# Performance work log

Hardware: AMD Instinct MI355X
Metric: run time of the kernel (lower is better)

Reference implementation:

```python
import jax, jax.numpy as jnp
import numpy as np

N, E, D, H = 20000, 320000, 128, 256
N_ITER = 3

def _w(k, fi, fo):
    return jax.random.normal(k, (fi, fo), jnp.float32) / np.sqrt(fi)

def setup_inputs() -> dict:
    key = jax.random.key(0)
    ks = jax.random.split(key, 16)
    inp = {
        "x": jax.random.normal(ks[0], (N, D), jnp.float32),
        "edge_attr": jax.random.normal(ks[1], (E, D), jnp.float32),
        "edge_index": jax.random.randint(ks[2], (2, E), 0, N, jnp.int32),
        # EASP edge encoder: cat[src,tgt,edge] (3D) -> H -> D
        "enc_w1": _w(ks[3], 3 * D, H), "enc_b1": jnp.zeros((H,), jnp.float32),
        "enc_w2": _w(ks[4], H, D), "enc_b2": jnp.zeros((D,), jnp.float32),
        # EdgeCNN: cat[src(2D), tgt(2D), edge(2D)] = 6D -> H -> D (reattach doubles dims)
        "em_w1": _w(ks[5], 6 * D, H), "em_b1": jnp.zeros((H,), jnp.float32),
        "em_w2": _w(ks[6], H, D), "em_b2": jnp.zeros((D,), jnp.float32),
        # node message MLP: cat[x_src(2D), edge(D)] = 3D -> H -> D
        "nm_w1": _w(ks[7], 3 * D, H), "nm_b1": jnp.zeros((H,), jnp.float32),
        "nm_w2": _w(ks[8], H, D), "nm_b2": jnp.zeros((D,), jnp.float32),
        # node output linear after aggregation
        "no_w": _w(ks[9], D, D), "no_b": jnp.zeros((D,), jnp.float32),
        # shared LayerNorms (ModuleList([layer]*n_iter) shares params)
        "node_ln_g": jnp.ones((D,), jnp.float32), "node_ln_b": jnp.zeros((D,), jnp.float32),
        "edge_ln_g": jnp.ones((D,), jnp.float32), "edge_ln_b": jnp.zeros((D,), jnp.float32),
    }
    return inp

def _ln(v, g, b):
    mu = jnp.mean(v, axis=-1, keepdims=True)
    var = jnp.mean(jnp.square(v - mu), axis=-1, keepdims=True)
    return (v - mu) * jax.lax.rsqrt(var + 1e-5) * g + b

def _mlp2(v, w1, b1, w2, b2):
    return jnp.maximum(v @ w1 + b1, 0.0) @ w2 + b2

def reference(x, edge_attr, edge_index,
              enc_w1, enc_b1, enc_w2, enc_b2,
              em_w1, em_b1, em_w2, em_b2,
              nm_w1, nm_b1, nm_w2, nm_b2,
              no_w, no_b, node_ln_g, node_ln_b, edge_ln_g, edge_ln_b):
    src, tgt = edge_index[0], edge_index[1]
    # edge encoder (EASP)
    init_edge = _mlp2(jnp.concatenate([x[src], x[tgt], edge_attr], axis=1),
                      enc_w1, enc_b1, enc_w2, enc_b2)  # [E, D]
    node_f, edge_f = x, init_edge
    deg = jax.ops.segment_sum(jnp.ones((E,), jnp.float32), tgt, num_segments=N)
    inv_deg = 1.0 / jnp.maximum(deg, 1.0)  # [N]
    for _ in range(N_ITER):
        node_c = jnp.concatenate([x, node_f], axis=1)          # [N, 2D] reattach
        edge_c = jnp.concatenate([init_edge, edge_f], axis=1)  # [E, 2D] reattach
        # edge update
        edge_f = _mlp2(jnp.concatenate([node_c[src], node_c[tgt], edge_c], axis=1),
                       em_w1, em_b1, em_w2, em_b2)             # [E, D]
        # node update: message -> scatter-mean -> linear
        msg = _mlp2(jnp.concatenate([node_c[src], edge_f], axis=1),
                    nm_w1, nm_b1, nm_w2, nm_b2)                # [E, D]
        agg = jax.ops.segment_sum(msg, tgt, num_segments=N) * inv_deg[:, None]
        node_f = agg @ no_w + no_b                             # [N, D]
        # residual + shared LayerNorm
        node_f = _ln(x + node_f, node_ln_g, node_ln_b)
        edge_f = _ln(init_edge + edge_f, edge_ln_g, edge_ln_b)
    return node_f, edge_f
```

## Files before the change

kernel.cpp:

```cpp
#include <hip/hip_runtime.h>
#include <stdint.h>

#define NN 20000
#define NE 320000
#define DD 128
#define HH 256
#define EB 48
#define EBE 64

using ushort8 = __attribute__((ext_vector_type(8))) unsigned short;
using bf16x8  = __attribute__((ext_vector_type(8))) __bf16;
using floatx4 = __attribute__((ext_vector_type(4))) float;

__device__ __forceinline__ unsigned short f2bf(float f) {
  union { float f; uint32_t u; } c; c.f = f;
  uint32_t u = c.u;
  return (unsigned short)((u + 0x7FFFu + ((u >> 16) & 1u)) >> 16);
}
__device__ __forceinline__ float bf2f(unsigned short h) {
  union { uint32_t u; float f; } c; c.u = ((uint32_t)h) << 16;
  return c.f;
}
__device__ __forceinline__ bf16x8 ld_bf8(const unsigned short* p) {
  ushort8 t = *(const ushort8*)p;
  return __builtin_bit_cast(bf16x8, t);
}
__device__ __forceinline__ void split8(const float* p, bf16x8& hi, bf16x8& lo) {
  floatx4 f0 = *(const floatx4*)p;
  floatx4 f1 = *(const floatx4*)(p + 4);
  ushort8 h, l;
#pragma unroll
  for (int k = 0; k < 4; ++k) {
    unsigned short a = f2bf(f0[k]);
    h[k] = a; l[k] = f2bf(f0[k] - bf2f(a));
    unsigned short b = f2bf(f1[k]);
    h[k+4] = b; l[k+4] = f2bf(f1[k] - bf2f(b));
  }
  hi = __builtin_bit_cast(bf16x8, h);
  lo = __builtin_bit_cast(bf16x8, l);
}
__device__ __forceinline__ floatx4 MFMA3(bf16x8 ah, bf16x8 al, bf16x8 bh, bf16x8 bl, floatx4 c) {
  c = __builtin_amdgcn_mfma_f32_16x16x32_bf16(ah, bh, c, 0, 0, 0);
  c = __builtin_amdgcn_mfma_f32_16x16x32_bf16(al, bh, c, 0, 0, 0);
  c = __builtin_amdgcn_mfma_f32_16x16x32_bf16(ah, bl, c, 0, 0, 0);
  return c;
}


__global__ void wconv_kernel(const float* __restrict__ in,
                             unsigned short* __restrict__ out_hi,
                             unsigned short* __restrict__ out_lo,
                             int K, int Nc) {
  int i = blockIdx.x * 256 + threadIdx.x;
  if (i >= K * Nc) return;
  int k = i / Nc, n = i - k * Nc;
  float v = in[i];
  unsigned short h = f2bf(v);
  out_hi[(size_t)n * K + k] = h;
  out_lo[(size_t)n * K + k] = f2bf(v - bf2f(h));
}

__global__ void xconv_kernel(const float* __restrict__ x,
                             unsigned short* __restrict__ xh, unsigned short* __restrict__ xl,
                             unsigned short* __restrict__ nh, unsigned short* __restrict__ nl) {
  int i = blockIdx.x * 256 + threadIdx.x;
  if (i < NN * DD) {
    float v = x[i];
    unsigned short h = f2bf(v), l = f2bf(v - bf2f(h));
    xh[i] = h; xl[i] = l; nh[i] = h; nl[i] = l;
  }
}

__global__ void deg_kernel(const int* __restrict__ ei, float* __restrict__ deg) {
  int e = blockIdx.x * 256 + threadIdx.x;
  if (e < NE) atomicAdd(&deg[ei[NE + e]], 1.0f);
}

__global__ void inv_kernel(const float* __restrict__ deg, float* __restrict__ idg) {
  int n = blockIdx.x * 256 + threadIdx.x;
  if (n < NN) idg[n] = 1.0f / fmaxf(deg[n], 1.0f);
}


template<int NCH, bool USE_NF>
__launch_bounds__(256, 2)
__global__ void nodepre_kernel(
    const unsigned short* __restrict__ xh, const unsigned short* __restrict__ xl,
    const unsigned short* __restrict__ nh, const unsigned short* __restrict__ nl,
    const unsigned short* __restrict__ w0h, const unsigned short* __restrict__ w0l,
    int ko0, int st0, float* __restrict__ out0,
    const unsigned short* __restrict__ w1h, const unsigned short* __restrict__ w1l,
    int ko1, int st1, float* __restrict__ out1,
    const unsigned short* __restrict__ w2h, const unsigned short* __restrict__ w2l,
    int ko2, int st2, float* __restrict__ out2)
{
  const int y = blockIdx.y;
  const unsigned short* Wh = (y == 0) ? w0h : (y == 1) ? w1h : w2h;
  const unsigned short* Wl = (y == 0) ? w0l : (y == 1) ? w1l : w2l;
  const int ko = (y == 0) ? ko0 : (y == 1) ? ko1 : ko2;
  const int st = (y == 0) ? st0 : (y == 1) ? st1 : st2;
  float* out = (y == 0) ? out0 : (y == 1) ? out1 : out2;

  const int tid = threadIdx.x;
  const int n0 = blockIdx.x * 64;
  const int lane = tid & 63, wv = tid >> 6;
  const int lr = lane & 15, kg = lane >> 4;
  int nr[4];
#pragma unroll
  for (int rt = 0; rt < 4; ++rt) {
    const int n = n0 + rt*16 + lr;
    nr[rt] = (n < NN) ? n : (NN - 1);
  }
  const floatx4 Z4 = {0.f, 0.f, 0.f, 0.f};
  floatx4 acc[4][4];
#pragma unroll
  for (int i = 0; i < 4; ++i)
#pragma unroll
    for (int j = 0; j < 4; ++j) acc[i][j] = Z4;

#pragma unroll
  for (int ch = 0; ch < NCH; ++ch) {
    bf16x8 ah[4], al[4], bh[4], bl[4];
#pragma unroll
    for (int rt = 0; rt < 4; ++rt) {
      if (USE_NF && ch >= 4) {
        const size_t off = (size_t)nr[rt] * DD + (ch - 4)*32 + kg*8;
        ah[rt] = ld_bf8(nh + off); al[rt] = ld_bf8(nl + off);
      } else {
        const size_t off = (size_t)nr[rt] * DD + ch*32 + kg*8;
        ah[rt] = ld_bf8(xh + off); al[rt] = ld_bf8(xl + off);
      }
    }
#pragma unroll
    for (int ct = 0; ct < 4; ++ct) {
      const size_t wo = (size_t)(wv*64 + ct*16 + lr) * st + ko + ch*32 + kg*8;
      bh[ct] = ld_bf8(Wh + wo); bl[ct] = ld_bf8(Wl + wo);
    }
#pragma unroll
    for (int rt = 0; rt < 4; ++rt)
#pragma unroll
      for (int ct = 0; ct < 4; ++ct) acc[rt][ct] = MFMA3(ah[rt], al[rt], bh[ct], bl[ct], acc[rt][ct]);
  }
#pragma unroll
  for (int ct = 0; ct < 4; ++ct) {
    const int col = wv*64 + ct*16 + lr;
#pragma unroll
    for (int rt = 0; rt < 4; ++rt)
#pragma unroll
      for (int j = 0; j < 4; ++j) {
        const int n = n0 + rt*16 + kg*4 + j;
        if (n < NN) out[(size_t)n * HH + col] = acc[rt][ct][j];
      }
  }
}


__launch_bounds__(256, 2)
__global__ void encoder_kernel(
    const float* __restrict__ ea,
    const int* __restrict__ ei,
    const float* __restrict__ pes,
    const float* __restrict__ pet,
    const unsigned short* __restrict__ w1h, const unsigned short* __restrict__ w1l,
    const float* __restrict__ b1,
    const unsigned short* __restrict__ w2h, const unsigned short* __restrict__ w2l,
    const float* __restrict__ b2,
    float* __restrict__ ief32, float* __restrict__ eff32)
{
  __shared__ unsigned short h_hi[EBE * 264];
  __shared__ unsigned short h_lo[EBE * 264];
  __shared__ int sidx[EBE];
  __shared__ int tidx[EBE];
  const int tid = threadIdx.x;
  const int e0 = blockIdx.x * EBE;
  if (tid < EBE) { sidx[tid] = ei[e0 + tid]; tidx[tid] = ei[NE + e0 + tid]; }
  __syncthreads();

  const int lane = tid & 63, wv = tid >> 6;
  const int lr = lane & 15, kg = lane >> 4;
  const floatx4 Z4 = {0.f, 0.f, 0.f, 0.f};

  float pse[4][4][4];
#pragma unroll
  for (int rt = 0; rt < 4; ++rt)
#pragma unroll
    for (int j = 0; j < 4; ++j) {
      const int row = rt*16 + kg*4 + j;
      const float* ps = pes + (size_t)sidx[row] * HH;
      const float* pt = pet + (size_t)tidx[row] * HH;
#pragma unroll
      for (int ct = 0; ct < 4; ++ct) {
        const int col = wv*64 + ct*16 + lr;
        pse[rt][j][ct] = ps[col] + pt[col];
      }
    }

  floatx4 acc[4][4];
#pragma unroll
  for (int i = 0; i < 4; ++i)
#pragma unroll
    for (int j = 0; j < 4; ++j) acc[i][j] = Z4;
#pragma unroll
  for (int sub = 0; sub < 4; ++sub) {
    const int off = sub*32 + kg*8;
    bf16x8 ah[4], al[4], bh[4], bl[4];
#pragma unroll
    for (int rt = 0; rt < 4; ++rt)
      split8(ea + (size_t)(e0 + rt*16 + lr) * DD + off, ah[rt], al[rt]);
#pragma unroll
    for (int ct = 0; ct < 4; ++ct) {
      const size_t wo = (size_t)(wv*64 + ct*16 + lr) * 384 + 256 + off;
      bh[ct] = ld_bf8(w1h + wo); bl[ct] = ld_bf8(w1l + wo);
    }
#pragma unroll
    for (int rt = 0; rt < 4; ++rt)
#pragma unroll
      for (int ct = 0; ct < 4; ++ct) acc[rt][ct] = MFMA3(ah[rt], al[rt], bh[ct], bl[ct], acc[rt][ct]);
  }
#pragma unroll
  for (int ct = 0; ct < 4; ++ct) {
    const int col = wv*64 + ct*16 + lr;
    const float bias = b1[col];
#pragma unroll
    for (int rt = 0; rt < 4; ++rt)
#pragma unroll
      for (int j = 0; j < 4; ++j) {
        const float v = fmaxf(acc[rt][ct][j] + bias + pse[rt][j][ct], 0.f);
        const unsigned short hh = f2bf(v);
        const int idx = (rt*16 + kg*4 + j) * 264 + col;
        h_hi[idx] = hh;
        h_lo[idx] = f2bf(v - bf2f(hh));
      }
  }
  __syncthreads();

  floatx4 acc2[4][2];
#pragma unroll
  for (int i = 0; i < 4; ++i) { acc2[i][0] = Z4; acc2[i][1] = Z4; }
#pragma unroll
  for (int ch = 0; ch < 8; ++ch) {
    bf16x8 ah[4], al[4], bh[2], bl[2];
#pragma unroll
    for (int rt = 0; rt < 4; ++rt) {
      const int idx = (rt*16 + lr) * 264 + ch*32 + kg*8;
      ah[rt] = ld_bf8(&h_hi[idx]); al[rt] = ld_bf8(&h_lo[idx]);
    }
#pragma unroll
    for (int c2 = 0; c2 < 2; ++c2) {
      const size_t wo = (size_t)(wv*32 + c2*16 + lr) * 256 + ch*32 + kg*8;
      bh[c2] = ld_bf8(w2h + wo); bl[c2] = ld_bf8(w2l + wo);
    }
#pragma unroll
    for (int rt = 0; rt < 4; ++rt)
#pragma unroll
      for (int c2 = 0; c2 < 2; ++c2) acc2[rt][c2] = MFMA3(ah[rt], al[rt], bh[c2], bl[c2], acc2[rt][c2]);
  }
#pragma unroll
  for (int c2 = 0; c2 < 2; ++c2) {
    const int col = wv*32 + c2*16 + lr;
    const float bias = b2[col];
#pragma unroll
    for (int rt = 0; rt < 4; ++rt)
#pragma unroll
      for (int j = 0; j < 4; ++j) {
        const float fv = acc2[rt][c2][j] + bias;
        const size_t idx = (size_t)(e0 + rt*16 + kg*4 + j) * DD + col;
        ief32[idx] = fv;
        eff32[idx] = fv;
      }
  }
}


__launch_bounds__(256, 2)
__global__ void edge_iter_kernel(
    const float* __restrict__ ief32,
    float* __restrict__ eff32,
    const int* __restrict__ ei,
    const float* __restrict__ pse_,
    const float* __restrict__ pte_,
    const float* __restrict__ psm_,
    const unsigned short* __restrict__ ew1h, const unsigned short* __restrict__ ew1l,
    const float* __restrict__ eb1,
    const unsigned short* __restrict__ ew2h, const unsigned short* __restrict__ ew2l,
    const float* __restrict__ eb2,
    const unsigned short* __restrict__ mw1h, const unsigned short* __restrict__ mw1l,
    const float* __restrict__ mb1,
    const unsigned short* __restrict__ mw2h, const unsigned short* __restrict__ mw2l,
    const float* __restrict__ mb2,
    const float* __restrict__ lng, const float* __restrict__ lnb,
    float* __restrict__ agg,
    float* __restrict__ out_edge,
    int write_out)
{
  __shared__ unsigned short h_hi[EB * 264];
  __shared__ unsigned short h_lo[EB * 264];
  __shared__ float eraw_f32[EB * 132];
  __shared__ int sidx[EB];
  __shared__ int tidx[EB];

  const int tid = threadIdx.x;
  const int e0 = blockIdx.x * EB;
  if (tid < EB) {
    const int e = e0 + tid;
    const int ec = (e < NE) ? e : (NE - 1);
    sidx[tid] = ei[ec];
    tidx[tid] = ei[NE + ec];
  }
  __syncthreads();

  const int lane = tid & 63, wv = tid >> 6;
  const int lr = lane & 15, kg = lane >> 4;
  int erow_c[3];
#pragma unroll
  for (int rt = 0; rt < 3; ++rt) {
    const int er = e0 + rt*16 + lr;
    erow_c[rt] = (er < NE) ? er : (NE - 1);
  }
  const floatx4 Z4 = {0.f, 0.f, 0.f, 0.f};

  float pse[3][4][4];
#pragma unroll
  for (int rt = 0; rt < 3; ++rt)
#pragma unroll
    for (int j = 0; j < 4; ++j) {
      const int row = rt*16 + kg*4 + j;
      const float* ps = pse_ + (size_t)sidx[row] * HH;
      const float* pt = pte_ + (size_t)tidx[row] * HH;
#pragma unroll
      for (int ct = 0; ct < 4; ++ct) {
        const int col = wv*64 + ct*16 + lr;
        pse[rt][j][ct] = ps[col] + pt[col];
      }
    }

  floatx4 acc[3][4];
#pragma unroll
  for (int i = 0; i < 3; ++i)
#pragma unroll
    for (int j = 0; j < 4; ++j) acc[i][j] = Z4;

#pragma unroll
  for (int seg = 0; seg < 2; ++seg) {
    const float* fb[3];
#pragma unroll
    for (int rt = 0; rt < 3; ++rt) {
      const size_t e = (size_t)erow_c[rt] * DD;
      fb[rt] = (seg == 0) ? ief32 + e : eff32 + e;
    }
#pragma unroll
    for (int sub = 0; sub < 4; ++sub) {
      const int off = sub*32 + kg*8;
      bf16x8 ah[3], al[3], bh[4], bl[4];
#pragma unroll
      for (int rt = 0; rt < 3; ++rt) split8(fb[rt] + off, ah[rt], al[rt]);
#pragma unroll
      for (int ct = 0; ct < 4; ++ct) {
        const size_t wo = (size_t)(wv*64 + ct*16 + lr) * 768 + 512 + seg*128 + off;
        bh[ct] = ld_bf8(ew1h + wo); bl[ct] = ld_bf8(ew1l + wo);
      }
#pragma unroll
      for (int rt = 0; rt < 3; ++rt)
#pragma unroll
        for (int ct = 0; ct < 4; ++ct) acc[rt][ct] = MFMA3(ah[rt], al[rt], bh[ct], bl[ct], acc[rt][ct]);
    }
  }
#pragma unroll
  for (int ct = 0; ct < 4; ++ct) {
    const int col = wv*64 + ct*16 + lr;
    const float bias = eb1[col];
#pragma unroll
    for (int rt = 0; rt < 3; ++rt)
#pragma unroll
      for (int j = 0; j < 4; ++j) {
        const float v = fmaxf(acc[rt][ct][j] + bias + pse[rt][j][ct], 0.f);
        const unsigned short hh = f2bf(v);
        const int idx = (rt*16 + kg*4 + j) * 264 + col;
        h_hi[idx] = hh;
        h_lo[idx] = f2bf(v - bf2f(hh));
      }
  }
  __syncthreads();

  floatx4 acc2[3][2];
#pragma unroll
  for (int i = 0; i < 3; ++i) { acc2[i][0] = Z4; acc2[i][1] = Z4; }
#pragma unroll
  for (int ch = 0; ch < 8; ++ch) {
    bf16x8 ah[3], al[3], bh[2], bl[2];
#pragma unroll
    for (int rt = 0; rt < 3; ++rt) {
      const int idx = (rt*16 + lr) * 264 + ch*32 + kg*8;
      ah[rt] = ld_bf8(&h_hi[idx]); al[rt] = ld_bf8(&h_lo[idx]);
    }
#pragma unroll
    for (int c2 = 0; c2 < 2; ++c2) {
      const size_t wo = (size_t)(wv*32 + c2*16 + lr) * 256 + ch*32 + kg*8;
      bh[c2] = ld_bf8(ew2h + wo); bl[c2] = ld_bf8(ew2l + wo);
    }
#pragma unroll
    for (int rt = 0; rt < 3; ++rt)
#pragma unroll
      for (int c2 = 0; c2 < 2; ++c2) acc2[rt][c2] = MFMA3(ah[rt], al[rt], bh[c2], bl[c2], acc2[rt][c2]);
  }
#pragma unroll
  for (int c2 = 0; c2 < 2; ++c2) {
    const int col = wv*32 + c2*16 + lr;
    const float bias = eb2[col];
#pragma unroll
    for (int rt = 0; rt < 3; ++rt)
#pragma unroll
      for (int j = 0; j < 4; ++j)
        eraw_f32[(rt*16 + kg*4 + j) * 132 + col] = acc2[rt][c2][j] + bias;
  }
  __syncthreads();

  float psm[3][4][4];
#pragma unroll
  for (int rt = 0; rt < 3; ++rt)
#pragma unroll
    for (int j = 0; j < 4; ++j) {
      const int row = rt*16 + kg*4 + j;
      const float* ps = psm_ + (size_t)sidx[row] * HH;
#pragma unroll
      for (int ct = 0; ct < 4; ++ct)
        psm[rt][j][ct] = ps[wv*64 + ct*16 + lr];
    }

  floatx4 accm[3][4];
#pragma unroll
  for (int i = 0; i < 3; ++i)
#pragma unroll
    for (int j = 0; j < 4; ++j) accm[i][j] = Z4;
#pragma unroll
  for (int sub = 0; sub < 4; ++sub) {
    const int off = sub*32 + kg*8;
    bf16x8 ah[3], al[3], bh[4], bl[4];
#pragma unroll
    for (int rt = 0; rt < 3; ++rt)
      split8(&eraw_f32[(rt*16 + lr) * 132 + off], ah[rt], al[rt]);
#pragma unroll
    for (int ct = 0; ct < 4; ++ct) {
      const size_t wo = (size_t)(wv*64 + ct*16 + lr) * 384 + 256 + off;
      bh[ct] = ld_bf8(mw1h + wo); bl[ct] = ld_bf8(mw1l + wo);
    }
#pragma unroll
    for (int rt = 0; rt < 3; ++rt)
#pragma unroll
      for (int ct = 0; ct < 4; ++ct) accm[rt][ct] = MFMA3(ah[rt], al[rt], bh[ct], bl[ct], accm[rt][ct]);
  }
#pragma unroll
  for (int ct = 0; ct < 4; ++ct) {
    const int col = wv*64 + ct*16 + lr;
    const float bias = mb1[col];
#pragma unroll
    for (int rt = 0; rt < 3; ++rt)
#pragma unroll
      for (int j = 0; j < 4; ++j) {
        const float v = fmaxf(accm[rt][ct][j] + bias + psm[rt][j][ct], 0.f);
        const unsigned short hh = f2bf(v);
        const int idx = (rt*16 + kg*4 + j) * 264 + col;
        h_hi[idx] = hh;
        h_lo[idx] = f2bf(v - bf2f(hh));
      }
  }
  __syncthreads();

  floatx4 accq[3][2];
#pragma unroll
  for (int i = 0; i < 3; ++i) { accq[i][0] = Z4; accq[i][1] = Z4; }
#pragma unroll
  for (int ch = 0; ch < 8; ++ch) {
    bf16x8 ah[3], al[3], bh[2], bl[2];
#pragma unroll
    for (int rt = 0; rt < 3; ++rt) {
      const int idx = (rt*16 + lr) * 264 + ch*32 + kg*8;
      ah[rt] = ld_bf8(&h_hi[idx]); al[rt] = ld_bf8(&h_lo[idx]);
    }
#pragma unroll
    for (int c2 = 0; c2 < 2; ++c2) {
      const size_t wo = (size_t)(wv*32 + c2*16 + lr) * 256 + ch*32 + kg*8;
      bh[c2] = ld_bf8(mw2h + wo); bl[c2] = ld_bf8(mw2l + wo);
    }
#pragma unroll
    for (int rt = 0; rt < 3; ++rt)
#pragma unroll
      for (int c2 = 0; c2 < 2; ++c2) accq[rt][c2] = MFMA3(ah[rt], al[rt], bh[c2], bl[c2], accq[rt][c2]);
  }
#pragma unroll
  for (int c2 = 0; c2 < 2; ++c2) {
    const int col = wv*32 + c2*16 + lr;
    const float bias = mb2[col];
#pragma unroll
    for (int rt = 0; rt < 3; ++rt)
#pragma unroll
      for (int j = 0; j < 4; ++j) {
        const int row = rt*16 + kg*4 + j;
        if (e0 + row < NE)
          atomicAdd(&agg[(size_t)tidx[row] * DD + col], accq[rt][c2][j] + bias);
      }
  }

  if (tid < EB * 4) {
    const int row = tid >> 2, sub = tid & 3;
    const int er = e0 + row;
    if (er < NE) {
      const size_t e = (size_t)er;
      float v[32];
      float s = 0.f, ss = 0.f;
#pragma unroll
      for (int c8 = 0; c8 < 4; ++c8) {
        const float* rp = &eraw_f32[row * 132 + sub*32 + c8*8];
        const float* ip = &ief32[e * DD + sub*32 + c8*8];
        floatx4 r0 = *(const floatx4*)rp;
        floatx4 r1 = *(const floatx4*)(rp + 4);
        floatx4 i0 = *(const floatx4*)ip;
        floatx4 i1 = *(const floatx4*)(ip + 4);
#pragma unroll
        for (int k = 0; k < 4; ++k) {
          float v0 = r0[k] + i0[k];
          float v1 = r1[k] + i1[k];
          v[c8*8 + k] = v0; v[c8*8 + 4 + k] = v1;
          s += v0 + v1; ss += v0*v0 + v1*v1;
        }
      }
      s  += __shfl_xor(s, 1);  s  += __shfl_xor(s, 2);
      ss += __shfl_xor(ss, 1); ss += __shfl_xor(ss, 2);
      const float mu  = s * (1.f/128.f);
      const float var = ss * (1.f/128.f) - mu * mu;
      const float inv = rsqrtf(fmaxf(var, 0.f) + 1e-5f);
#pragma unroll
      for (int c8 = 0; c8 < 4; ++c8) {
        floatx4 o0, o1;
#pragma unroll
        for (int k = 0; k < 8; ++k) {
          const int col = sub*32 + c8*8 + k;
          const float o = (v[c8*8 + k] - mu) * inv * lng[col] + lnb[col];
          if (k < 4) o0[k] = o; else o1[k-4] = o;
        }
        *(floatx4*)&eff32[e * DD + sub*32 + c8*8] = o0;
        *(floatx4*)&eff32[e * DD + sub*32 + c8*8 + 4] = o1;
        if (write_out) {
          *(floatx4*)&out_edge[e * DD + sub*32 + c8*8] = o0;
          *(floatx4*)&out_edge[e * DD + sub*32 + c8*8 + 4] = o1;
        }
      }
    }
  }
}


__launch_bounds__(256, 2)
__global__ void node_update_kernel(
    const float* __restrict__ agg, const float* __restrict__ idg,
    const unsigned short* __restrict__ nwh, const unsigned short* __restrict__ nwl,
    const float* __restrict__ nb,
    const float* __restrict__ x,
    const float* __restrict__ lng, const float* __restrict__ lnb,
    float* __restrict__ out_node,
    unsigned short* __restrict__ nh, unsigned short* __restrict__ nl,
    int write_out)
{
  __shared__ unsigned short a_hi[64 * 136];
  __shared__ unsigned short a_lo[64 * 136];
  __shared__ float o_lds[64 * 132];
  const int tid = threadIdx.x;
  const int n0 = blockIdx.x * 64;
  const int row = tid >> 2, sub = tid & 3;
  const int n = n0 + row;
  {
    const float s = (n < NN) ? idg[n] : 0.f;
#pragma unroll
    for (int c4 = 0; c4 < 8; ++c4) {
      floatx4 v = {0.f, 0.f, 0.f, 0.f};
      if (n < NN) v = *(const floatx4*)&agg[(size_t)n * DD + sub*32 + c4*4];
#pragma unroll
      for (int k = 0; k < 4; ++k) {
        const float f = v[k] * s;
        const unsigned short hh = f2bf(f);
        const int idx = row * 136 + sub*32 + c4*4 + k;
        a_hi[idx] = hh;
        a_lo[idx] = f2bf(f - bf2f(hh));
      }
    }
  }
  __syncthreads();

  const int lane = tid & 63, wv = tid >> 6;
  const int lr = lane & 15, kg = lane >> 4;
  const floatx4 Z4 = {0.f, 0.f, 0.f, 0.f};
  floatx4 acc[4][2];
#pragma unroll
  for (int i = 0; i < 4; ++i) { acc[i][0] = Z4; acc[i][1] = Z4; }
#pragma unroll
  for (int ch = 0; ch < 4; ++ch) {
    bf16x8 ah[4], al[4], bh[2], bl[2];
#pragma unroll
    for (int rt = 0; rt < 4; ++rt) {
      const int idx = (rt*16 + lr) * 136 + ch*32 + kg*8;
      ah[rt] = ld_bf8(&a_hi[idx]); al[rt] = ld_bf8(&a_lo[idx]);
    }
#pragma unroll
    for (int c2 = 0; c2 < 2; ++c2) {
      const size_t wo = (size_t)(wv*32 + c2*16 + lr) * DD + ch*32 + kg*8;
      bh[c2] = ld_bf8(nwh + wo); bl[c2] = ld_bf8(nwl + wo);
    }
#pragma unroll
    for (int rt = 0; rt < 4; ++rt)
#pragma unroll
      for (int c2 = 0; c2 < 2; ++c2) acc[rt][c2] = MFMA3(ah[rt], al[rt], bh[c2], bl[c2], acc[rt][c2]);
  }
#pragma unroll
  for (int c2 = 0; c2 < 2; ++c2) {
    const int col = wv*32 + c2*16 + lr;
    const float bias = nb[col];
#pragma unroll
    for (int rt = 0; rt < 4; ++rt)
#pragma unroll
      for (int j = 0; j < 4; ++j)
        o_lds[(rt*16 + kg*4 + j) * 132 + col] = acc[rt][c2][j] + bias;
  }
  __syncthreads();

  if (n < NN) {
    float v[32];
    float s = 0.f, ss = 0.f;
#pragma unroll
    for (int c4 = 0; c4 < 8; ++c4) {
      floatx4 xa = *(const floatx4*)&x[(size_t)n * DD + sub*32 + c4*4];
#pragma unroll
      for (int k = 0; k < 4; ++k) {
        const float val = o_lds[row * 132 + sub*32 + c4*4 + k] + xa[k];
        v[c4*4 + k] = val; s += val; ss += val * val;
      }
    }
    s  += __shfl_xor(s, 1);  s  += __shfl_xor(s, 2);
    ss += __shfl_xor(ss, 1); ss += __shfl_xor(ss, 2);
    const float mu  = s * (1.f/128.f);
    const float var = ss * (1.f/128.f) - mu * mu;
    const float inv = rsqrtf(fmaxf(var, 0.f) + 1e-5f);
#pragma unroll
    for (int c8 = 0; c8 < 4; ++c8) {
      floatx4 o0, o1; ushort8 oh, ol;
#pragma unroll
      for (int k = 0; k < 8; ++k) {
        const int col = sub*32 + c8*8 + k;
        const float o = (v[c8*8 + k] - mu) * inv * lng[col] + lnb[col];
        if (k < 4) o0[k] = o; else o1[k-4] = o;
        const unsigned short hh = f2bf(o);
        oh[k] = hh;
        ol[k] = f2bf(o - bf2f(hh));
      }
      if (write_out) {
        *(floatx4*)&out_node[(size_t)n * DD + sub*32 + c8*8] = o0;
        *(floatx4*)&out_node[(size_t)n * DD + sub*32 + c8*8 + 4] = o1;
      }
      *(ushort8*)&nh[(size_t)n * DD + sub*32 + c8*8] = oh;
      *(ushort8*)&nl[(size_t)n * DD + sub*32 + c8*8] = ol;
    }
  }
}


extern "C" void kernel_launch(void* const* d_in, const int* in_sizes, int n_in,
                              void* d_out, int out_size, void* d_ws, size_t ws_size,
                              hipStream_t stream) {
  (void)in_sizes; (void)n_in; (void)out_size; (void)ws_size;

  const float* x      = (const float*)d_in[0];
  const float* ea     = (const float*)d_in[1];
  const int*   ei     = (const int*)d_in[2];
  const float* enc_w1 = (const float*)d_in[3];
  const float* enc_b1 = (const float*)d_in[4];
  const float* enc_w2 = (const float*)d_in[5];
  const float* enc_b2 = (const float*)d_in[6];
  const float* em_w1  = (const float*)d_in[7];
  const float* em_b1  = (const float*)d_in[8];
  const float* em_w2  = (const float*)d_in[9];
  const float* em_b2  = (const float*)d_in[10];
  const float* nm_w1  = (const float*)d_in[11];
  const float* nm_b1  = (const float*)d_in[12];
  const float* nm_w2  = (const float*)d_in[13];
  const float* nm_b2  = (const float*)d_in[14];
  const float* no_w   = (const float*)d_in[15];
  const float* no_b   = (const float*)d_in[16];
  const float* nlng   = (const float*)d_in[17];
  const float* nlnb   = (const float*)d_in[18];
  const float* elng   = (const float*)d_in[19];
  const float* elnb   = (const float*)d_in[20];

  float* out_node = (float*)d_out;
  float* ief32    = out_node + (size_t)NN * DD;

  char* p = (char*)d_ws;
  auto alloc = [&](size_t bytes) -> void* {
    void* r = (void*)p;
    p += (bytes + 255) & ~(size_t)255;
    return r;
  };
  unsigned short* xb_h = (unsigned short*)alloc((size_t)NN * DD * 2);
  unsigned short* xb_l = (unsigned short*)alloc((size_t)NN * DD * 2);
  unsigned short* nf_h = (unsigned short*)alloc((size_t)NN * DD * 2);
  unsigned short* nf_l = (unsigned short*)alloc((size_t)NN * DD * 2);
  float*          eff32 = (float*)alloc((size_t)NE * DD * 4);
  float*          agg  = (float*)alloc((size_t)NN * DD * 4);
  float*          deg  = (float*)alloc((size_t)NN * 4);
  float*          idg  = (float*)alloc((size_t)NN * 4);
  float*          psrc_e = (float*)alloc((size_t)NN * HH * 4);
  float*          ptgt_e = (float*)alloc((size_t)NN * HH * 4);
  float*          psrc_m = (float*)alloc((size_t)NN * HH * 4);
  unsigned short* cw1h = (unsigned short*)alloc((size_t)384 * 256 * 2);
  unsigned short* cw1l = (unsigned short*)alloc((size_t)384 * 256 * 2);
  unsigned short* cw2h = (unsigned short*)alloc((size_t)256 * 128 * 2);
  unsigned short* cw2l = (unsigned short*)alloc((size_t)256 * 128 * 2);
  unsigned short* ew1h = (unsigned short*)alloc((size_t)768 * 256 * 2);
  unsigned short* ew1l = (unsigned short*)alloc((size_t)768 * 256 * 2);
  unsigned short* ew2h = (unsigned short*)alloc((size_t)256 * 128 * 2);
  unsigned short* ew2l = (unsigned short*)alloc((size_t)256 * 128 * 2);
  unsigned short* mw1h = (unsigned short*)alloc((size_t)384 * 256 * 2);
  unsigned short* mw1l = (unsigned short*)alloc((size_t)384 * 256 * 2);
  unsigned short* mw2h = (unsigned short*)alloc((size_t)256 * 128 * 2);
  unsigned short* mw2l = (unsigned short*)alloc((size_t)256 * 128 * 2);
  unsigned short* nwh  = (unsigned short*)alloc((size_t)128 * 128 * 2);
  unsigned short* nwl  = (unsigned short*)alloc((size_t)128 * 128 * 2);

  wconv_kernel<<<(384*256 + 255)/256, 256, 0, stream>>>(enc_w1, cw1h, cw1l, 384, 256);
  wconv_kernel<<<(256*128 + 255)/256, 256, 0, stream>>>(enc_w2, cw2h, cw2l, 256, 128);
  wconv_kernel<<<(768*256 + 255)/256, 256, 0, stream>>>(em_w1, ew1h, ew1l, 768, 256);
  wconv_kernel<<<(256*128 + 255)/256, 256, 0, stream>>>(em_w2, ew2h, ew2l, 256, 128);
  wconv_kernel<<<(384*256 + 255)/256, 256, 0, stream>>>(nm_w1, mw1h, mw1l, 384, 256);
  wconv_kernel<<<(256*128 + 255)/256, 256, 0, stream>>>(nm_w2, mw2h, mw2l, 256, 128);
  wconv_kernel<<<(128*128 + 255)/256, 256, 0, stream>>>(no_w, nwh, nwl, 128, 128);

  xconv_kernel<<<(NN*DD + 255)/256, 256, 0, stream>>>(x, xb_h, xb_l, nf_h, nf_l);

  hipMemsetAsync(deg, 0, (size_t)NN * 4, stream);
  deg_kernel<<<(NE + 255)/256, 256, 0, stream>>>(ei, deg);
  inv_kernel<<<(NN + 255)/256, 256, 0, stream>>>(deg, idg);

  nodepre_kernel<4, false><<<dim3(313, 2), 256, 0, stream>>>(
      xb_h, xb_l, nf_h, nf_l,
      cw1h, cw1l, 0,   384, psrc_e,
      cw1h, cw1l, 128, 384, ptgt_e,
      cw1h, cw1l, 0,   384, psrc_e);

  encoder_kernel<<<NE/EBE, 256, 0, stream>>>(ea, ei, psrc_e, ptgt_e,
                                             cw1h, cw1l, enc_b1, cw2h, cw2l, enc_b2,
                                             ief32, eff32);

  const int egrid = (NE + EB - 1) / EB;
  for (int it = 0; it < 3; ++it) {
    const int last = (it == 2) ? 1 : 0;
    nodepre_kernel<8, true><<<dim3(313, 3), 256, 0, stream>>>(
        xb_h, xb_l, nf_h, nf_l,
        ew1h, ew1l, 0,   768, psrc_e,
        ew1h, ew1l, 256, 768, ptgt_e,
        mw1h, mw1l, 0,   384, psrc_m);
    hipMemsetAsync(agg, 0, (size_t)NN * DD * 4, stream);
    edge_iter_kernel<<<egrid, 256, 0, stream>>>(
        ief32, eff32, ei, psrc_e, ptgt_e, psrc_m,
        ew1h, ew1l, em_b1, ew2h, ew2l, em_b2,
        mw1h, mw1l, nm_b1, mw2h, mw2l, nm_b2,
        elng, elnb, agg, ief32, last);
    node_update_kernel<<<(NN + 63)/64, 256, 0, stream>>>(
        agg, idg, nwh, nwl, no_b, x, nlng, nlnb, out_node, nf_h, nf_l, last);
  }
}
```

Before: 3.423 ms.

## Sort edges by source node and keep edge features in sorted order

Adds a counting sort of edges by source index (histogram, scan, scatter) and stores init and running edge features in source-sorted order. Edge-iteration blocks then process consecutive edges that share source nodes, so the per-source projection gathers are more likely to hit cache. A final unsort kernel scatters the edge output back to the original order. The cost is a few setup kernels plus an extra full pass over the edge feature array, while target gathers and the aggregation atomics stay random.

```diff
diff --git a/kernel.cpp b/kernel.cpp
--- a/kernel.cpp
+++ b/kernel.cpp
@@ -79,6 +79,62 @@
 __global__ void inv_kernel(const float* __restrict__ deg, float* __restrict__ idg) {
   int n = blockIdx.x * 256 + threadIdx.x;
   if (n < NN) idg[n] = 1.0f / fmaxf(deg[n], 1.0f);
+}
+
+
+__global__ void hist_kernel(const int* __restrict__ ei, int* __restrict__ hist) {
+  int e = blockIdx.x * 256 + threadIdx.x;
+  if (e < NE) atomicAdd(&hist[ei[e]], 1);
+}
+
+__global__ void scan_kernel(const int* __restrict__ hist,
+                            int* __restrict__ offset, int* __restrict__ cursor) {
+  __shared__ int tot[256];
+  __shared__ int pre[256];
+  const int t = threadIdx.x;
+  const int CH = (NN + 255) / 256;
+  const int c0 = t * CH;
+  int s = 0;
+  for (int i = 0; i < CH; ++i) {
+    int b = c0 + i;
+    if (b < NN) s += hist[b];
+  }
+  tot[t] = s;
+  __syncthreads();
+  if (t == 0) {
+    int acc = 0;
+    for (int i = 0; i < 256; ++i) { pre[i] = acc; acc += tot[i]; }
+  }
+  __syncthreads();
+  int acc = pre[t];
+  for (int i = 0; i < CH; ++i) {
+    int b = c0 + i;
+    if (b < NN) { offset[b] = acc; cursor[b] = acc; acc += hist[b]; }
+  }
+}
+
+__global__ void scatter_kernel(const int* __restrict__ ei, int* __restrict__ cursor,
+                               int* __restrict__ sord, int* __restrict__ rank,
+                               int* __restrict__ ssrc, int* __restrict__ stgt) {
+  int e = blockIdx.x * 256 + threadIdx.x;
+  if (e < NE) {
+    const int s = ei[e];
+    const int pos = atomicAdd(&cursor[s], 1);
+    sord[pos] = e;
+    rank[e]  = pos;
+    ssrc[pos] = s;
+    stgt[pos] = ei[NE + e];
+  }
+}
+
+__global__ void unsort_kernel(const float* __restrict__ efs, const int* __restrict__ sord,
+                              float* __restrict__ out_edge) {
+  int i = blockIdx.x * 256 + threadIdx.x;
+  if (i < NE * 32) {
+    const int p = i >> 5, c4 = i & 31;
+    floatx4 v = *(const floatx4*)&efs[(size_t)p * DD + c4 * 4];
+    *(floatx4*)&out_edge[(size_t)sord[p] * DD + c4 * 4] = v;
+  }
 }
 
 
@@ -159,21 +215,27 @@
 __global__ void encoder_kernel(
     const float* __restrict__ ea,
     const int* __restrict__ ei,
+    const int* __restrict__ rank,
     const float* __restrict__ pes,
     const float* __restrict__ pet,
     const unsigned short* __restrict__ w1h, const unsigned short* __restrict__ w1l,
     const float* __restrict__ b1,
     const unsigned short* __restrict__ w2h, const unsigned short* __restrict__ w2l,
     const float* __restrict__ b2,
-    float* __restrict__ ief32, float* __restrict__ eff32)
+    float* __restrict__ ie_srt, float* __restrict__ ef_srt)
 {
   __shared__ unsigned short h_hi[EBE * 264];
   __shared__ unsigned short h_lo[EBE * 264];
   __shared__ int sidx[EBE];
   __shared__ int tidx[EBE];
+  __shared__ int rk[EBE];
   const int tid = threadIdx.x;
   const int e0 = blockIdx.x * EBE;
-  if (tid < EBE) { sidx[tid] = ei[e0 + tid]; tidx[tid] = ei[NE + e0 + tid]; }
+  if (tid < EBE) {
+    sidx[tid] = ei[e0 + tid];
+    tidx[tid] = ei[NE + e0 + tid];
+    rk[tid]   = rank[e0 + tid];
+  }
   __syncthreads();
 
   const int lane = tid & 63, wv = tid >> 6;
@@ -264,9 +326,9 @@
 #pragma unroll
       for (int j = 0; j < 4; ++j) {
         const float fv = acc2[rt][c2][j] + bias;
-        const size_t idx = (size_t)(e0 + rt*16 + kg*4 + j) * DD + col;
-        ief32[idx] = fv;
-        eff32[idx] = fv;
+        const size_t sp = (size_t)rk[rt*16 + kg*4 + j];
+        ie_srt[sp * DD + col] = fv;
+        ef_srt[sp * DD + col] = fv;
       }
   }
 }
@@ -274,9 +336,10 @@
 
 __launch_bounds__(256, 2)
 __global__ void edge_iter_kernel(
-    const float* __restrict__ ief32,
-    float* __restrict__ eff32,
-    const int* __restrict__ ei,
+    const float* __restrict__ ie_srt,
+    float* __restrict__ ef_srt,
+    const int* __restrict__ ssrc,
+    const int* __restrict__ stgt,
     const float* __restrict__ pse_,
     const float* __restrict__ pte_,
     const float* __restrict__ psm_,
@@ -289,33 +352,31 @@
     const unsigned short* __restrict__ mw2h, const unsigned short* __restrict__ mw2l,
     const float* __restrict__ mb2,
     const float* __restrict__ lng, const float* __restrict__ lnb,
-    float* __restrict__ agg,
-    float* __restrict__ out_edge,
-    int write_out)
+    float* __restrict__ agg)
 {
   __shared__ unsigned short h_hi[EB * 264];
   __shared__ unsigned short h_lo[EB * 264];
   __shared__ float eraw_f32[EB * 132];
-  __shared__ int sidx[EB];
-  __shared__ int tidx[EB];
+  __shared__ int s_lds[EB];
+  __shared__ int t_lds[EB];
 
   const int tid = threadIdx.x;
-  const int e0 = blockIdx.x * EB;
+  const int p0 = blockIdx.x * EB;
   if (tid < EB) {
-    const int e = e0 + tid;
-    const int ec = (e < NE) ? e : (NE - 1);
-    sidx[tid] = ei[ec];
-    tidx[tid] = ei[NE + ec];
+    const int p = p0 + tid;
+    const int pc = (p < NE) ? p : (NE - 1);
+    s_lds[tid] = ssrc[pc];
+    t_lds[tid] = stgt[pc];
   }
   __syncthreads();
 
   const int lane = tid & 63, wv = tid >> 6;
   const int lr = lane & 15, kg = lane >> 4;
-  int erow_c[3];
+  int prow_c[3];
 #pragma unroll
   for (int rt = 0; rt < 3; ++rt) {
-    const int er = e0 + rt*16 + lr;
-    erow_c[rt] = (er < NE) ? er : (NE - 1);
+    const int p = p0 + rt*16 + lr;
+    prow_c[rt] = (p < NE) ? p : (NE - 1);
   }
   const floatx4 Z4 = {0.f, 0.f, 0.f, 0.f};
 
@@ -325,8 +386,8 @@
 #pragma unroll
     for (int j = 0; j < 4; ++j) {
       const int row = rt*16 + kg*4 + j;
-      const float* ps = pse_ + (size_t)sidx[row] * HH;
-      const float* pt = pte_ + (size_t)tidx[row] * HH;
+      const float* ps = pse_ + (size_t)s_lds[row] * HH;
+      const float* pt = pte_ + (size_t)t_lds[row] * HH;
 #pragma unroll
       for (int ct = 0; ct < 4; ++ct) {
         const int col = wv*64 + ct*16 + lr;
@@ -345,8 +406,8 @@
     const float* fb[3];
 #pragma unroll
     for (int rt = 0; rt < 3; ++rt) {
-      const size_t e = (size_t)erow_c[rt] * DD;
-      fb[rt] = (seg == 0) ? ief32 + e : eff32 + e;
+      const size_t e = (size_t)prow_c[rt] * DD;
+      fb[rt] = (seg == 0) ? ie_srt + e : ef_srt + e;
     }
 #pragma unroll
     for (int sub = 0; sub < 4; ++sub) {
@@ -421,7 +482,7 @@
 #pragma unroll
     for (int j = 0; j < 4; ++j) {
       const int row = rt*16 + kg*4 + j;
-      const float* ps = psm_ + (size_t)sidx[row] * HH;
+      const float* ps = psm_ + (size_t)s_lds[row] * HH;
 #pragma unroll
       for (int ct = 0; ct < 4; ++ct)
         psm[rt][j][ct] = ps[wv*64 + ct*16 + lr];
@@ -496,22 +557,22 @@
 #pragma unroll
       for (int j = 0; j < 4; ++j) {
         const int row = rt*16 + kg*4 + j;
-        if (e0 + row < NE)
-          atomicAdd(&agg[(size_t)tidx[row] * DD + col], accq[rt][c2][j] + bias);
+        if (p0 + row < NE)
+          atomicAdd(&agg[(size_t)t_lds[row] * DD + col], accq[rt][c2][j] + bias);
       }
   }
 
   if (tid < EB * 4) {
     const int row = tid >> 2, sub = tid & 3;
-    const int er = e0 + row;
-    if (er < NE) {
-      const size_t e = (size_t)er;
+    const int p = p0 + row;
+    if (p < NE) {
+      const size_t e = (size_t)p;
       float v[32];
       float s = 0.f, ss = 0.f;
 #pragma unroll
       for (int c8 = 0; c8 < 4; ++c8) {
         const float* rp = &eraw_f32[row * 132 + sub*32 + c8*8];
-        const float* ip = &ief32[e * DD + sub*32 + c8*8];
+        const float* ip = &ie_srt[e * DD + sub*32 + c8*8];
         floatx4 r0 = *(const floatx4*)rp;
         floatx4 r1 = *(const floatx4*)(rp + 4);
         floatx4 i0 = *(const floatx4*)ip;
@@ -538,12 +599,8 @@
           const float o = (v[c8*8 + k] - mu) * inv * lng[col] + lnb[col];
           if (k < 4) o0[k] = o; else o1[k-4] = o;
         }
-        *(floatx4*)&eff32[e * DD + sub*32 + c8*8] = o0;
-        *(floatx4*)&eff32[e * DD + sub*32 + c8*8 + 4] = o1;
-        if (write_out) {
-          *(floatx4*)&out_edge[e * DD + sub*32 + c8*8] = o0;
-          *(floatx4*)&out_edge[e * DD + sub*32 + c8*8 + 4] = o1;
-        }
+        *(floatx4*)&ef_srt[e * DD + sub*32 + c8*8] = o0;
+        *(floatx4*)&ef_srt[e * DD + sub*32 + c8*8 + 4] = o1;
       }
     }
   }
@@ -690,7 +747,7 @@
   const float* elnb   = (const float*)d_in[20];
 
   float* out_node = (float*)d_out;
-  float* ief32    = out_node + (size_t)NN * DD;
+  float* ie_srt   = out_node + (size_t)NN * DD;
 
   char* p = (char*)d_ws;
   auto alloc = [&](size_t bytes) -> void* {
@@ -702,13 +759,20 @@
   unsigned short* xb_l = (unsigned short*)alloc((size_t)NN * DD * 2);
   unsigned short* nf_h = (unsigned short*)alloc((size_t)NN * DD * 2);
   unsigned short* nf_l = (unsigned short*)alloc((size_t)NN * DD * 2);
-  float*          eff32 = (float*)alloc((size_t)NE * DD * 4);
+  float*          ef_srt = (float*)alloc((size_t)NE * DD * 4);
   float*          agg  = (float*)alloc((size_t)NN * DD * 4);
   float*          deg  = (float*)alloc((size_t)NN * 4);
   float*          idg  = (float*)alloc((size_t)NN * 4);
   float*          psrc_e = (float*)alloc((size_t)NN * HH * 4);
   float*          ptgt_e = (float*)alloc((size_t)NN * HH * 4);
   float*          psrc_m = (float*)alloc((size_t)NN * HH * 4);
+  int*            hist   = (int*)alloc((size_t)NN * 4);
+  int*            offset = (int*)alloc((size_t)NN * 4);
+  int*            cursor = (int*)alloc((size_t)NN * 4);
+  int*            sord   = (int*)alloc((size_t)NE * 4);
+  int*            rank   = (int*)alloc((size_t)NE * 4);
+  int*            ssrc   = (int*)alloc((size_t)NE * 4);
+  int*            stgt   = (int*)alloc((size_t)NE * 4);
   unsigned short* cw1h = (unsigned short*)alloc((size_t)384 * 256 * 2);
   unsigned short* cw1l = (unsigned short*)alloc((size_t)384 * 256 * 2);
   unsigned short* cw2h = (unsigned short*)alloc((size_t)256 * 128 * 2);
@@ -738,15 +802,20 @@
   deg_kernel<<<(NE + 255)/256, 256, 0, stream>>>(ei, deg);
   inv_kernel<<<(NN + 255)/256, 256, 0, stream>>>(deg, idg);
 
+  hipMemsetAsync(hist, 0, (size_t)NN * 4, stream);
+  hist_kernel<<<(NE + 255)/256, 256, 0, stream>>>(ei, hist);
+  scan_kernel<<<1, 256, 0, stream>>>(hist, offset, cursor);
+  scatter_kernel<<<(NE + 255)/256, 256, 0, stream>>>(ei, cursor, sord, rank, ssrc, stgt);
+
   nodepre_kernel<4, false><<<dim3(313, 2), 256, 0, stream>>>(
       xb_h, xb_l, nf_h, nf_l,
       cw1h, cw1l, 0,   384, psrc_e,
       cw1h, cw1l, 128, 384, ptgt_e,
       cw1h, cw1l, 0,   384, psrc_e);
 
-  encoder_kernel<<<NE/EBE, 256, 0, stream>>>(ea, ei, psrc_e, ptgt_e,
+  encoder_kernel<<<NE/EBE, 256, 0, stream>>>(ea, ei, rank, psrc_e, ptgt_e,
                                              cw1h, cw1l, enc_b1, cw2h, cw2l, enc_b2,
-                                             ief32, eff32);
+                                             ie_srt, ef_srt);
 
   const int egrid = (NE + EB - 1) / EB;
   for (int it = 0; it < 3; ++it) {
@@ -758,11 +827,13 @@
         mw1h, mw1l, 0,   384, psrc_m);
     hipMemsetAsync(agg, 0, (size_t)NN * DD * 4, stream);
     edge_iter_kernel<<<egrid, 256, 0, stream>>>(
-        ief32, eff32, ei, psrc_e, ptgt_e, psrc_m,
+        ie_srt, ef_srt, ssrc, stgt, psrc_e, ptgt_e, psrc_m,
         ew1h, ew1l, em_b1, ew2h, ew2l, em_b2,
         mw1h, mw1l, nm_b1, mw2h, mw2l, nm_b2,
-        elng, elnb, agg, ief32, last);
+        elng, elnb, agg);
     node_update_kernel<<<(NN + 63)/64, 256, 0, stream>>>(
         agg, idg, nwh, nwl, no_b, x, nlng, nlnb, out_node, nf_h, nf_l, last);
   }
-}
+
+  unsort_kernel<<<(NE*32 + 255)/256, 256, 0, stream>>>(ef_srt, sord, ie_srt);
+}
```

Result: slower. 3.537 ms (+3.3%).
